# Performance work log

Measured on AMD Instinct MI355X. Metric: run time of the kernel, lower is better.

The kernel has to match this reference:

```python
import jax, jax.numpy as jnp
import numpy as np

K = 16            # n_keypoint
B = 32            # batch
N = 16384         # points per cloud
P = K * (K - 1) // 2  # 120 decoder pairs

_PAIRS_I = np.array([i for i in range(K) for j in range(i)])
_PAIRS_J = np.array([j for i in range(K) for j in range(i)])


def _batchnorm(x, g, b):
    # torch BatchNorm1d in training mode: batch stats, biased var, eps=1e-5
    mu = jnp.mean(x, axis=0)
    var = jnp.mean((x - mu) ** 2, axis=0)
    return g * (x - mu) / jnp.sqrt(var + 1e-5) + b


def _kpcd(input_x, KP, ptl_w, ptl_b):
    KPL = KP @ ptl_w + ptl_b                                  # [B,N,K]
    KPA = jax.nn.softmax(jnp.transpose(KPL, (0, 2, 1)), axis=-1)  # [B,K,N]
    KPCD = jnp.einsum('bkn,bnd->bkd', KPA, input_x)           # [B,K,3]
    return KPA, KPCD


def _counts(KPCD):
    # host-side replica of the .item() sync: count = min(200, max(15, int(dist/0.01)))
    A = KPCD[:, _PAIRS_I, :]
    Bp = KPCD[:, _PAIRS_J, :]
    dists = jnp.mean(jnp.sqrt(0.001 + jnp.sum((A - Bp) ** 2, -1)), axis=0)  # [P]
    return np.clip((np.asarray(dists) / 0.01).astype(np.int32), 15, 200)


def setup_inputs() -> dict:
    key = jax.random.key(0)
    ks = jax.random.split(key, 9)
    f32 = jnp.float32
    return {
        'input_x': jax.random.normal(ks[0], (B, N, 3), f32),
        'KP': jax.random.normal(ks[1], (B, N, K), f32),
        'GF': jax.random.normal(ks[2], (B, 1024, 16), f32),
        'ptl_w': jax.random.normal(ks[3], (K, K), f32) * 0.25,   # PT_L weight [in,out]
        'ptl_b': jnp.zeros((K,), f32),
        'ma_w1': jax.random.normal(ks[4], (1024, 512), f32) * 0.03,
        'ma_b1': jnp.zeros((512,), f32),
        'bn1_g': jnp.ones((512,), f32),
        'bn1_b': jnp.zeros((512,), f32),
        'ma_w2': jax.random.normal(ks[5], (512, 256), f32) * 0.04,
        'ma_b2': jnp.zeros((256,), f32),
        'bn2_g': jnp.ones((256,), f32),
        'bn2_b': jnp.zeros((256,), f32),
        'mal_w': jax.random.normal(ks[6], (256, P), f32) * 0.06,
        'mal_b': jnp.zeros((P,), f32),
        'emb': jax.random.normal(ks[7], (P, 200, 3), f32) * 0.002,  # per-pair DecoderUnit emb
    }


def reference(input_x, KP, GF, ptl_w, ptl_b, ma_w1, ma_b1, bn1_g, bn1_b,
              ma_w2, ma_b2, bn2_g, bn2_b, mal_w, mal_b, emb):
    KPA, KPCD = _kpcd(input_x, KP, ptl_w, ptl_b)
    counts = _counts(KPCD)
    A = KPCD[:, _PAIRS_I, :]   # [B,P,3]
    Bp = KPCD[:, _PAIRS_J, :]  # [B,P,3]
    RP = []
    for p in range(P):  # small fixed pair loop (120), data dims vectorized
        c = int(counts[p])
        f = jnp.linspace(0.0, 1.0, c)[None, :, None]       # [1,c,1]
        Kc = A[:, p, None, :] * f + Bp[:, p, None, :] * (1.0 - f)  # [B,c,3]
        RP.append(emb[p, :c][None, :, :] + Kc)
    RP_concat = jnp.concatenate(RP, axis=1)  # [B, sum(counts), 3]

    GFP = jnp.max(GF, axis=-1)  # max_pool1d(GF,16).squeeze(-1) -> [B,1024]
    h = jax.nn.relu(_batchnorm(GFP @ ma_w1 + ma_b1, bn1_g, bn1_b))
    h = jax.nn.relu(_batchnorm(h @ ma_w2 + ma_b2, bn2_g, bn2_b))
    MA = jax.nn.sigmoid(h @ mal_w + mal_b)   # [B,P]

    LF = jnp.transpose(emb, (1, 0, 2)).reshape(200, P * 3)  # torch.cat(L, dim=1)
    return (RP_concat, KPCD, KPA, LF, MA)
```

## Files before the change

kernel.cpp:

```cpp
#include <hip/hip_runtime.h>

#define B_ 32
#define N_ 16384
#define K_ 16
#define P_ 120
#define CH_ 32
#define PTS 512
#define ITERS 8

__global__ __launch_bounds__(256) void k_main(const float* __restrict__ KP,
                                              const float* __restrict__ W,
                                              float* __restrict__ out_kpa,
                                              float* __restrict__ parts,
                                              const float* __restrict__ emb,
                                              float* __restrict__ out_lf,
                                              const float* __restrict__ GF,
                                              float* __restrict__ gfp) {
    int bid = blockIdx.x, t = threadIdx.x;
    if (bid >= 1024) {
        if (bid < 1306) {
            int i = (bid - 1024) * 256 + t;
            if (i < 200 * P_ * 3) {
                int cc = i / (P_ * 3);
                int r = i - cc * (P_ * 3);
                int p = r / 3, d = r - 3 * p;
                out_lf[i] = emb[((size_t)p * 200 + cc) * 3 + d];
            }
        } else {
            int i = (bid - 1306) * 256 + t;
            const float4* g = (const float4*)(GF + (size_t)i * 16);
            float4 a = g[0], b = g[1], c = g[2], d = g[3];
            float m = fmaxf(fmaxf(fmaxf(a.x, a.y), fmaxf(a.z, a.w)),
                            fmaxf(fmaxf(b.x, b.y), fmaxf(b.z, b.w)));
            m = fmaxf(m, fmaxf(fmaxf(c.x, c.y), fmaxf(c.z, c.w)));
            m = fmaxf(m, fmaxf(fmaxf(d.x, d.y), fmaxf(d.z, d.w)));
            gfp[i] = m;
        }
        return;
    }
    int ch = bid & (CH_ - 1), b = bid >> 5;
    int w = t >> 6, q = t & 3;
    __shared__ float Wl[256];
    Wl[t] = W[t];
    __syncthreads();
    float Wr[4][4][4];
#pragma unroll
    for (int m = 0; m < 4; ++m)
#pragma unroll
        for (int jj = 0; jj < 4; ++jj)
#pragma unroll
            for (int kk = 0; kk < 4; ++kk)
                Wr[m][jj][kk] = Wl[(4 * (q ^ m) + jj) * 16 + 4 * q + kk];
    const float4* KP4 = (const float4*)KP;
    size_t base = (size_t)b * (N_ * 4) + (size_t)ch * (PTS * 4);
    float s4[4] = {0.0f, 0.0f, 0.0f, 0.0f};
#pragma unroll
    for (int it = 0; it < ITERS; ++it) {
        float4 a = KP4[base + it * 256 + t];
        float c0 = __shfl_xor(a.x, 1), c1 = __shfl_xor(a.y, 1), c2 = __shfl_xor(a.z, 1), c3 = __shfl_xor(a.w, 1);
        float d0 = __shfl_xor(a.x, 2), d1 = __shfl_xor(a.y, 2), d2 = __shfl_xor(a.z, 2), d3 = __shfl_xor(a.w, 2);
        float e0 = __shfl_xor(a.x, 3), e1 = __shfl_xor(a.y, 3), e2 = __shfl_xor(a.z, 3), e3 = __shfl_xor(a.w, 3);
        int n = ch * PTS + it * 64 + (t >> 2);
#pragma unroll
        for (int kk = 0; kk < 4; ++kk) {
            float v = a.x * Wr[0][0][kk];
            v = fmaf(a.y, Wr[0][1][kk], v); v = fmaf(a.z, Wr[0][2][kk], v); v = fmaf(a.w, Wr[0][3][kk], v);
            v = fmaf(c0, Wr[1][0][kk], v);  v = fmaf(c1, Wr[1][1][kk], v);
            v = fmaf(c2, Wr[1][2][kk], v);  v = fmaf(c3, Wr[1][3][kk], v);
            v = fmaf(d0, Wr[2][0][kk], v);  v = fmaf(d1, Wr[2][1][kk], v);
            v = fmaf(d2, Wr[2][2][kk], v);  v = fmaf(d3, Wr[2][3][kk], v);
            v = fmaf(e0, Wr[3][0][kk], v);  v = fmaf(e1, Wr[3][1][kk], v);
            v = fmaf(e2, Wr[3][2][kk], v);  v = fmaf(e3, Wr[3][3][kk], v);
            float ev = expf(v);
            out_kpa[((size_t)b * 16 + 4 * q + kk) * N_ + n] = ev;
            s4[kk] += ev;
        }
    }
#pragma unroll
    for (int o = 4; o <= 32; o <<= 1)
#pragma unroll
        for (int kk = 0; kk < 4; ++kk) s4[kk] += __shfl_xor(s4[kk], o);
    __shared__ float ss[4][4][4];
    if ((t & 63) < 4)
#pragma unroll
        for (int kk = 0; kk < 4; ++kk) ss[w][q][kk] = s4[kk];
    __syncthreads();
    if (t < 16) {
        int qq = t >> 2, kk = t & 3;
        parts[((size_t)b * 16 + t) * CH_ + ch] =
            ss[0][qq][kk] + ss[1][qq][kk] + ss[2][qq][kk] + ss[3][qq][kk];
    }
}

template<int INNER, int COLS, int SLICES>
__device__ __forceinline__ void mm_bn(const float* __restrict__ A, const float* __restrict__ W,
                                      const float* __restrict__ bias, const float* __restrict__ g,
                                      const float* __restrict__ bta, float* __restrict__ out,
                                      int col, int t, float (*red)[32]) {
    constexpr int PER = INNER / SLICES;
    int r = t & 31, s = t >> 5;
    const float4* a4 = (const float4*)(A + (size_t)r * INNER + s * PER);
    const float* wp = W + (size_t)(s * PER) * COLS + col;
    float acc = 0.0f;
#pragma unroll
    for (int j = 0; j < PER / 4; ++j) {
        float4 av = a4[j];
        acc = fmaf(av.x, wp[(size_t)(4 * j + 0) * COLS], acc);
        acc = fmaf(av.y, wp[(size_t)(4 * j + 1) * COLS], acc);
        acc = fmaf(av.z, wp[(size_t)(4 * j + 2) * COLS], acc);
        acc = fmaf(av.w, wp[(size_t)(4 * j + 3) * COLS], acc);
    }
    red[s][r] = acc;
    __syncthreads();
    if (s == 0) {
        float v = red[0][r];
#pragma unroll
        for (int qx = 1; qx < SLICES; ++qx) v += red[qx][r];
        v += bias[col];
        float mu = v;
#pragma unroll
        for (int o = 1; o <= 16; o <<= 1) mu += __shfl_xor(mu, o);
        mu *= (1.0f / 32.0f);
        float dd = v - mu, sq = dd * dd;
#pragma unroll
        for (int o = 1; o <= 16; o <<= 1) sq += __shfl_xor(sq, o);
        float var = sq * (1.0f / 32.0f);
        float y = g[col] * dd / sqrtf(var + 1e-5f) + bta[col];
        out[(size_t)r * COLS + col] = fmaxf(0.0f, y);
    }
}

__global__ __launch_bounds__(256) void k_scale(float* __restrict__ kpa,
                                               const float* __restrict__ parts,
                                               const float* __restrict__ X,
                                               float* __restrict__ kpcdpart,
                                               const float* __restrict__ gfp,
                                               const float* __restrict__ ma_w1,
                                               const float* __restrict__ ma_b1,
                                               const float* __restrict__ bn1_g,
                                               const float* __restrict__ bn1_b,
                                               float* __restrict__ h1n) {
    __shared__ float iSs[16];
    __shared__ float4 xs4[PTS * 3 / 4];
    __shared__ float red[8][32];
    int bid = blockIdx.x, t = threadIdx.x, w = t >> 6;
    if (bid >= 1024) {
        mm_bn<1024, 512, 8>(gfp, ma_w1, ma_b1, bn1_g, bn1_b, h1n, bid - 1024, t, red);
        return;
    }
    int ch = bid & (CH_ - 1), b = bid >> 5;
    if (t < 16) {
        const float* ps = parts + ((size_t)b * 16 + t) * CH_;
        double S = 0.0;
        for (int c2 = 0; c2 < CH_; ++c2) S += (double)ps[c2];
        iSs[t] = (float)(1.0 / S);
    }
    {
        const float4* X4 = (const float4*)X;
        size_t xb4 = (size_t)b * (N_ * 3 / 4) + (size_t)ch * (PTS * 3 / 4);
        for (int i = t; i < PTS * 3 / 4; i += 256) xs4[i] = X4[xb4 + i];
    }
    __syncthreads();
    const float* xs = (const float*)xs4;
    float4* kpa4 = (float4*)kpa;
    float acc[8][3];
#pragma unroll
    for (int kk = 0; kk < 8; ++kk)
#pragma unroll
        for (int d = 0; d < 3; ++d) acc[kk][d] = 0.0f;
    int half = t >> 7, off = t & 127;
#pragma unroll
    for (int kk = 0; kk < 8; ++kk) {
        int k = 2 * kk + half;
        float iS = iSs[k];
        size_t a4 = ((size_t)b * 16 + k) * (N_ / 4) + (size_t)ch * (PTS / 4) + off;
        float4 ev = kpa4[a4];
        float4 y = make_float4(ev.x * iS, ev.y * iS, ev.z * iS, ev.w * iS);
        kpa4[a4] = y;
        int p0 = off * 4;
        acc[kk][0] = fmaf(y.x, xs[(p0 + 0) * 3 + 0], acc[kk][0]);
        acc[kk][1] = fmaf(y.x, xs[(p0 + 0) * 3 + 1], acc[kk][1]);
        acc[kk][2] = fmaf(y.x, xs[(p0 + 0) * 3 + 2], acc[kk][2]);
        acc[kk][0] = fmaf(y.y, xs[(p0 + 1) * 3 + 0], acc[kk][0]);
        acc[kk][1] = fmaf(y.y, xs[(p0 + 1) * 3 + 1], acc[kk][1]);
        acc[kk][2] = fmaf(y.y, xs[(p0 + 1) * 3 + 2], acc[kk][2]);
        acc[kk][0] = fmaf(y.z, xs[(p0 + 2) * 3 + 0], acc[kk][0]);
        acc[kk][1] = fmaf(y.z, xs[(p0 + 2) * 3 + 1], acc[kk][1]);
        acc[kk][2] = fmaf(y.z, xs[(p0 + 2) * 3 + 2], acc[kk][2]);
        acc[kk][0] = fmaf(y.w, xs[(p0 + 3) * 3 + 0], acc[kk][0]);
        acc[kk][1] = fmaf(y.w, xs[(p0 + 3) * 3 + 1], acc[kk][1]);
        acc[kk][2] = fmaf(y.w, xs[(p0 + 3) * 3 + 2], acc[kk][2]);
    }
#pragma unroll
    for (int o = 1; o <= 32; o <<= 1)
#pragma unroll
        for (int kk = 0; kk < 8; ++kk)
#pragma unroll
            for (int d = 0; d < 3; ++d) acc[kk][d] += __shfl_xor(acc[kk][d], o);
    __shared__ float sacc[4][8][3];
    if ((t & 63) == 0)
#pragma unroll
        for (int kk = 0; kk < 8; ++kk)
#pragma unroll
            for (int d = 0; d < 3; ++d) sacc[w][kk][d] = acc[kk][d];
    __syncthreads();
    if (t < 48) {
        int k = t / 3, d = t - 3 * (t / 3);
        int kk = k >> 1;
        int w0 = (k & 1) ? 2 : 0;
        float s = sacc[w0][kk][d] + sacc[w0 + 1][kk][d];
        kpcdpart[(((size_t)b * 16 + k) * CH_ + ch) * 3 + d] = s;
    }
}

__global__ __launch_bounds__(256) void k_rp(const float* __restrict__ kpcdpart,
                                            const float* __restrict__ emb,
                                            float* __restrict__ out_rp,
                                            float* __restrict__ out_kpcd, int total,
                                            const float* __restrict__ h1n,
                                            const float* __restrict__ ma_w2,
                                            const float* __restrict__ ma_b2,
                                            const float* __restrict__ bn2_g,
                                            const float* __restrict__ bn2_b,
                                            float* __restrict__ h2n) {
    __shared__ double sKp[512 * 3];
    __shared__ int sc[P_], soffs[P_];
    __shared__ float red[8][32];
    int t = threadIdx.x, p = blockIdx.x;
    if (p >= 120) {
        mm_bn<512, 256, 8>(h1n, ma_w2, ma_b2, bn2_g, bn2_b, h2n, p - 120, t, red);
        return;
    }
    for (int bk = t; bk < 512; bk += 256) {
        for (int d = 0; d < 3; ++d) {
            double s = 0.0;
            for (int ch = 0; ch < CH_; ++ch)
                s += (double)kpcdpart[((size_t)bk * CH_ + ch) * 3 + d];
            sKp[bk * 3 + d] = s;
        }
    }
    __syncthreads();
    if (t < P_) {
        int pi = 1, base = 0;
        while (t >= base + pi) { base += pi; ++pi; }
        int pj = t - base;
        double accd = 0.0;
        for (int b = 0; b < B_; ++b) {
            const double* A  = sKp + ((size_t)b * K_ + pi) * 3;
            const double* Bp = sKp + ((size_t)b * K_ + pj) * 3;
            double dx = A[0] - Bp[0], dy = A[1] - Bp[1], dz = A[2] - Bp[2];
            accd += sqrt(0.001 + dx * dx + dy * dy + dz * dz);
        }
        double dist = accd / 32.0;
        int c = (int)(dist / 0.01);
        sc[t] = min(200, max(15, c));
    }
    __syncthreads();
    if (t == 0) {
        int o = 0;
        for (int qx = 0; qx < P_; ++qx) { soffs[qx] = o; o += sc[qx]; }
    }
    __syncthreads();
    if (p == 0) {
        for (int i = t; i < 1536; i += 256) out_kpcd[i] = (float)sKp[i];
    }
    int pi = 1, base = 0;
    while (p >= base + pi) { base += pi; ++pi; }
    int pj = p - base;
    int c = sc[p], off = soffs[p];
    float delta = 1.0f / (float)(c - 1);
    int per_b = c * 3;
    int nitems = B_ * per_b;
    size_t total3 = (size_t)total * 3;
    for (int i = t; i < nitems; i += 256) {
        int b = i / per_b;
        int r = i - b * per_b;
        int ii = r / 3, d = r - 3 * ii;
        float f = (float)ii * delta;
        float A  = (float)sKp[((size_t)b * K_ + pi) * 3 + d];
        float Bv = (float)sKp[((size_t)b * K_ + pj) * 3 + d];
        out_rp[(size_t)b * total3 + (size_t)(off + ii) * 3 + d] =
            emb[((size_t)p * 200 + ii) * 3 + d] + (A * f + Bv * (1.0f - f));
    }
}

template<int INNER, int COLS, int SLICES>
__global__ void k_mmsig(const float* __restrict__ A, const float* __restrict__ W,
                        const float* __restrict__ bias, float* __restrict__ out) {
    constexpr int PER = INNER / SLICES;
    int col = blockIdx.x;
    int t = threadIdx.x;
    int r = t & 31, s = t >> 5;
    const float4* a4 = (const float4*)(A + (size_t)r * INNER + s * PER);
    const float* wp = W + (size_t)(s * PER) * COLS + col;
    float acc = 0.0f;
#pragma unroll
    for (int j = 0; j < PER / 4; ++j) {
        float4 av = a4[j];
        acc = fmaf(av.x, wp[(size_t)(4 * j + 0) * COLS], acc);
        acc = fmaf(av.y, wp[(size_t)(4 * j + 1) * COLS], acc);
        acc = fmaf(av.z, wp[(size_t)(4 * j + 2) * COLS], acc);
        acc = fmaf(av.w, wp[(size_t)(4 * j + 3) * COLS], acc);
    }
    __shared__ float red[SLICES][32];
    red[s][r] = acc;
    __syncthreads();
    if (s == 0) {
        float v = red[0][r];
#pragma unroll
        for (int qx = 1; qx < SLICES; ++qx) v += red[qx][r];
        v += bias[col];
        out[(size_t)r * COLS + col] = 1.0f / (1.0f + expf(-v));
    }
}

extern "C" void kernel_launch(void* const* d_in, const int* in_sizes, int n_in,
                              void* d_out, int out_size, void* d_ws, size_t ws_size,
                              hipStream_t stream) {
    const float* input_x = (const float*)d_in[0];
    const float* KP      = (const float*)d_in[1];
    const float* GF      = (const float*)d_in[2];
    const float* ptl_w   = (const float*)d_in[3];
    const float* ma_w1   = (const float*)d_in[5];
    const float* ma_b1   = (const float*)d_in[6];
    const float* bn1_g   = (const float*)d_in[7];
    const float* bn1_b   = (const float*)d_in[8];
    const float* ma_w2   = (const float*)d_in[9];
    const float* ma_b2   = (const float*)d_in[10];
    const float* bn2_g   = (const float*)d_in[11];
    const float* bn2_b   = (const float*)d_in[12];
    const float* mal_w   = (const float*)d_in[13];
    const float* mal_b   = (const float*)d_in[14];
    const float* emb     = (const float*)d_in[15];

    float* out = (float*)d_out;
    size_t rp_elems = (size_t)out_size - 8465984ull;
    int total = (int)(rp_elems / 96ull);
    float* out_rp   = out;
    float* out_kpcd = out + rp_elems;
    float* out_kpa  = out_kpcd + 1536;
    float* out_lf   = out_kpa + 8388608ull;
    float* out_ma   = out_lf + 72000;

    char* w = (char*)d_ws;
    float*  parts    = (float*)(w + 1024);
    float*  kpcdpart = (float*)(w + 66560);
    float*  gfp      = (float*)(w + 263168);
    float*  h1n      = (float*)(w + 394240);
    float*  h2n      = (float*)(w + 459776);

    k_main <<<1434, 256, 0, stream>>>(KP, ptl_w, out_kpa, parts, emb, out_lf, GF, gfp);
    k_scale<<<1536, 256, 0, stream>>>(out_kpa, parts, input_x, kpcdpart,
                                      gfp, ma_w1, ma_b1, bn1_g, bn1_b, h1n);
    k_rp   <<<376, 256, 0, stream>>>(kpcdpart, emb, out_rp, out_kpcd, total,
                                     h1n, ma_w2, ma_b2, bn2_g, bn2_b, h2n);
    k_mmsig<256, 120, 4><<<120, 128, 0, stream>>>(h2n, mal_w, mal_b, out_ma);
}
```

Baseline: 62.98 us.

## Recompute softmax logits in second pass instead of storing and rereading exp

The stats kernel now only accumulates per-chunk exp sums without writing unnormalized values. The apply kernel rereads KP, recomputes the 16x16 projection and exp, scales by the inverse sum, writes KPA once, and accumulates KPCD directly using X loaded per point. This removes one full write and one read of the large KPA tensor, at the cost of duplicated matmul/exp compute and uncoalesced strided X loads.

```diff
diff --git a/kernel.cpp b/kernel.cpp
--- a/kernel.cpp
+++ b/kernel.cpp
@@ -8,14 +8,13 @@
 #define PTS 512
 #define ITERS 8
 
-__global__ __launch_bounds__(256) void k_main(const float* __restrict__ KP,
-                                              const float* __restrict__ W,
-                                              float* __restrict__ out_kpa,
-                                              float* __restrict__ parts,
-                                              const float* __restrict__ emb,
-                                              float* __restrict__ out_lf,
-                                              const float* __restrict__ GF,
-                                              float* __restrict__ gfp) {
+__global__ __launch_bounds__(256) void k_stats(const float* __restrict__ KP,
+                                               const float* __restrict__ W,
+                                               float* __restrict__ parts,
+                                               const float* __restrict__ emb,
+                                               float* __restrict__ out_lf,
+                                               const float* __restrict__ GF,
+                                               float* __restrict__ gfp) {
     int bid = blockIdx.x, t = threadIdx.x;
     if (bid >= 1024) {
         if (bid < 1306) {
@@ -60,7 +59,6 @@
         float c0 = __shfl_xor(a.x, 1), c1 = __shfl_xor(a.y, 1), c2 = __shfl_xor(a.z, 1), c3 = __shfl_xor(a.w, 1);
         float d0 = __shfl_xor(a.x, 2), d1 = __shfl_xor(a.y, 2), d2 = __shfl_xor(a.z, 2), d3 = __shfl_xor(a.w, 2);
         float e0 = __shfl_xor(a.x, 3), e1 = __shfl_xor(a.y, 3), e2 = __shfl_xor(a.z, 3), e3 = __shfl_xor(a.w, 3);
-        int n = ch * PTS + it * 64 + (t >> 2);
 #pragma unroll
         for (int kk = 0; kk < 4; ++kk) {
             float v = a.x * Wr[0][0][kk];
@@ -71,9 +69,7 @@
             v = fmaf(d2, Wr[2][2][kk], v);  v = fmaf(d3, Wr[2][3][kk], v);
             v = fmaf(e0, Wr[3][0][kk], v);  v = fmaf(e1, Wr[3][1][kk], v);
             v = fmaf(e2, Wr[3][2][kk], v);  v = fmaf(e3, Wr[3][3][kk], v);
-            float ev = expf(v);
-            out_kpa[((size_t)b * 16 + 4 * q + kk) * N_ + n] = ev;
-            s4[kk] += ev;
+            s4[kk] += expf(v);
         }
     }
 #pragma unroll
@@ -130,9 +126,11 @@
     }
 }
 
-__global__ __launch_bounds__(256) void k_scale(float* __restrict__ kpa,
+__global__ __launch_bounds__(256) void k_apply(const float* __restrict__ KP,
+                                               const float* __restrict__ W,
                                                const float* __restrict__ parts,
                                                const float* __restrict__ X,
+                                               float* __restrict__ out_kpa,
                                                float* __restrict__ kpcdpart,
                                                const float* __restrict__ gfp,
                                                const float* __restrict__ ma_w1,
@@ -140,75 +138,87 @@
                                                const float* __restrict__ bn1_g,
                                                const float* __restrict__ bn1_b,
                                                float* __restrict__ h1n) {
+    __shared__ float Wl[256];
     __shared__ float iSs[16];
-    __shared__ float4 xs4[PTS * 3 / 4];
     __shared__ float red[8][32];
-    int bid = blockIdx.x, t = threadIdx.x, w = t >> 6;
+    int bid = blockIdx.x, t = threadIdx.x;
     if (bid >= 1024) {
         mm_bn<1024, 512, 8>(gfp, ma_w1, ma_b1, bn1_g, bn1_b, h1n, bid - 1024, t, red);
         return;
     }
     int ch = bid & (CH_ - 1), b = bid >> 5;
+    int w = t >> 6, q = t & 3;
+    Wl[t] = W[t];
     if (t < 16) {
         const float* ps = parts + ((size_t)b * 16 + t) * CH_;
         double S = 0.0;
         for (int c2 = 0; c2 < CH_; ++c2) S += (double)ps[c2];
         iSs[t] = (float)(1.0 / S);
     }
-    {
-        const float4* X4 = (const float4*)X;
-        size_t xb4 = (size_t)b * (N_ * 3 / 4) + (size_t)ch * (PTS * 3 / 4);
-        for (int i = t; i < PTS * 3 / 4; i += 256) xs4[i] = X4[xb4 + i];
-    }
-    __syncthreads();
-    const float* xs = (const float*)xs4;
-    float4* kpa4 = (float4*)kpa;
-    float acc[8][3];
-#pragma unroll
-    for (int kk = 0; kk < 8; ++kk)
+    __syncthreads();
+    float Wr[4][4][4];
+#pragma unroll
+    for (int m = 0; m < 4; ++m)
+#pragma unroll
+        for (int jj = 0; jj < 4; ++jj)
+#pragma unroll
+            for (int kk = 0; kk < 4; ++kk)
+                Wr[m][jj][kk] = Wl[(4 * (q ^ m) + jj) * 16 + 4 * q + kk];
+    float iS[4];
+#pragma unroll
+    for (int kk = 0; kk < 4; ++kk) iS[kk] = iSs[4 * q + kk];
+    const float4* KP4 = (const float4*)KP;
+    size_t base = (size_t)b * (N_ * 4) + (size_t)ch * (PTS * 4);
+    float acc[4][3];
+#pragma unroll
+    for (int kk = 0; kk < 4; ++kk)
 #pragma unroll
         for (int d = 0; d < 3; ++d) acc[kk][d] = 0.0f;
-    int half = t >> 7, off = t & 127;
-#pragma unroll
-    for (int kk = 0; kk < 8; ++kk) {
-        int k = 2 * kk + half;
-        float iS = iSs[k];
-        size_t a4 = ((size_t)b * 16 + k) * (N_ / 4) + (size_t)ch * (PTS / 4) + off;
-        float4 ev = kpa4[a4];
-        float4 y = make_float4(ev.x * iS, ev.y * iS, ev.z * iS, ev.w * iS);
-        kpa4[a4] = y;
-        int p0 = off * 4;
-        acc[kk][0] = fmaf(y.x, xs[(p0 + 0) * 3 + 0], acc[kk][0]);
-        acc[kk][1] = fmaf(y.x, xs[(p0 + 0) * 3 + 1], acc[kk][1]);
-        acc[kk][2] = fmaf(y.x, xs[(p0 + 0) * 3 + 2], acc[kk][2]);
-        acc[kk][0] = fmaf(y.y, xs[(p0 + 1) * 3 + 0], acc[kk][0]);
-        acc[kk][1] = fmaf(y.y, xs[(p0 + 1) * 3 + 1], acc[kk][1]);
-        acc[kk][2] = fmaf(y.y, xs[(p0 + 1) * 3 + 2], acc[kk][2]);
-        acc[kk][0] = fmaf(y.z, xs[(p0 + 2) * 3 + 0], acc[kk][0]);
-        acc[kk][1] = fmaf(y.z, xs[(p0 + 2) * 3 + 1], acc[kk][1]);
-        acc[kk][2] = fmaf(y.z, xs[(p0 + 2) * 3 + 2], acc[kk][2]);
-        acc[kk][0] = fmaf(y.w, xs[(p0 + 3) * 3 + 0], acc[kk][0]);
-        acc[kk][1] = fmaf(y.w, xs[(p0 + 3) * 3 + 1], acc[kk][1]);
-        acc[kk][2] = fmaf(y.w, xs[(p0 + 3) * 3 + 2], acc[kk][2]);
-    }
-#pragma unroll
-    for (int o = 1; o <= 32; o <<= 1)
-#pragma unroll
-        for (int kk = 0; kk < 8; ++kk)
+    const float* xb = X + (size_t)b * N_ * 3;
+#pragma unroll
+    for (int it = 0; it < ITERS; ++it) {
+        float4 a = KP4[base + it * 256 + t];
+        float c0 = __shfl_xor(a.x, 1), c1 = __shfl_xor(a.y, 1), c2 = __shfl_xor(a.z, 1), c3 = __shfl_xor(a.w, 1);
+        float d0 = __shfl_xor(a.x, 2), d1 = __shfl_xor(a.y, 2), d2 = __shfl_xor(a.z, 2), d3 = __shfl_xor(a.w, 2);
+        float e0 = __shfl_xor(a.x, 3), e1 = __shfl_xor(a.y, 3), e2 = __shfl_xor(a.z, 3), e3 = __shfl_xor(a.w, 3);
+        int n = ch * PTS + it * 64 + (t >> 2);
+        float x0 = xb[(size_t)n * 3 + 0];
+        float x1 = xb[(size_t)n * 3 + 1];
+        float x2 = xb[(size_t)n * 3 + 2];
+#pragma unroll
+        for (int kk = 0; kk < 4; ++kk) {
+            float v = a.x * Wr[0][0][kk];
+            v = fmaf(a.y, Wr[0][1][kk], v); v = fmaf(a.z, Wr[0][2][kk], v); v = fmaf(a.w, Wr[0][3][kk], v);
+            v = fmaf(c0, Wr[1][0][kk], v);  v = fmaf(c1, Wr[1][1][kk], v);
+            v = fmaf(c2, Wr[1][2][kk], v);  v = fmaf(c3, Wr[1][3][kk], v);
+            v = fmaf(d0, Wr[2][0][kk], v);  v = fmaf(d1, Wr[2][1][kk], v);
+            v = fmaf(d2, Wr[2][2][kk], v);  v = fmaf(d3, Wr[2][3][kk], v);
+            v = fmaf(e0, Wr[3][0][kk], v);  v = fmaf(e1, Wr[3][1][kk], v);
+            v = fmaf(e2, Wr[3][2][kk], v);  v = fmaf(e3, Wr[3][3][kk], v);
+            float y = expf(v) * iS[kk];
+            out_kpa[((size_t)b * 16 + 4 * q + kk) * N_ + n] = y;
+            acc[kk][0] = fmaf(y, x0, acc[kk][0]);
+            acc[kk][1] = fmaf(y, x1, acc[kk][1]);
+            acc[kk][2] = fmaf(y, x2, acc[kk][2]);
+        }
+    }
+#pragma unroll
+    for (int o = 4; o <= 32; o <<= 1)
+#pragma unroll
+        for (int kk = 0; kk < 4; ++kk)
 #pragma unroll
             for (int d = 0; d < 3; ++d) acc[kk][d] += __shfl_xor(acc[kk][d], o);
-    __shared__ float sacc[4][8][3];
-    if ((t & 63) == 0)
-#pragma unroll
-        for (int kk = 0; kk < 8; ++kk)
-#pragma unroll
-            for (int d = 0; d < 3; ++d) sacc[w][kk][d] = acc[kk][d];
+    __shared__ float sa[4][4][4][3];
+    if ((t & 63) < 4)
+#pragma unroll
+        for (int kk = 0; kk < 4; ++kk)
+#pragma unroll
+            for (int d = 0; d < 3; ++d) sa[w][q][kk][d] = acc[kk][d];
     __syncthreads();
     if (t < 48) {
         int k = t / 3, d = t - 3 * (t / 3);
-        int kk = k >> 1;
-        int w0 = (k & 1) ? 2 : 0;
-        float s = sacc[w0][kk][d] + sacc[w0 + 1][kk][d];
+        int qq = k >> 2, kk = k & 3;
+        float s = sa[0][qq][kk][d] + sa[1][qq][kk][d] + sa[2][qq][kk][d] + sa[3][qq][kk][d];
         kpcdpart[(((size_t)b * 16 + k) * CH_ + ch) * 3 + d] = s;
     }
 }
@@ -349,8 +359,8 @@
     float*  h1n      = (float*)(w + 394240);
     float*  h2n      = (float*)(w + 459776);
 
-    k_main <<<1434, 256, 0, stream>>>(KP, ptl_w, out_kpa, parts, emb, out_lf, GF, gfp);
-    k_scale<<<1536, 256, 0, stream>>>(out_kpa, parts, input_x, kpcdpart,
+    k_stats<<<1434, 256, 0, stream>>>(KP, ptl_w, parts, emb, out_lf, GF, gfp);
+    k_apply<<<1536, 256, 0, stream>>>(KP, ptl_w, parts, input_x, out_kpa, kpcdpart,
                                       gfp, ma_w1, ma_b1, bn1_g, bn1_b, h1n);
     k_rp   <<<376, 256, 0, stream>>>(kpcdpart, emb, out_rp, out_kpcd, total,
                                      h1n, ma_w2, ma_b2, bn2_g, bn2_b, h2n);
```

New measurement: 58.95 us. 6.4% less time.
